# Kernel optimization log

Measured on AMD Instinct MI355X. Metric: run time of the kernel, lower is better.

The kernel has to match this reference:

```python
import jax, jax.numpy as jnp
import numpy as np

B, T, D_MODEL, N_HEADS = 2, 2048, 2048, 16
D_HEAD = D_MODEL // N_HEADS
SCALE = 1.0 / np.sqrt(D_HEAD)


def setup_inputs() -> dict:
    key = jax.random.key(0)
    ks = jax.random.split(key, 5)
    w_std = 1.0 / np.sqrt(D_MODEL)
    x = jax.random.normal(ks[0], (B, T, D_MODEL), dtype=jnp.float32)
    W_q = jax.random.normal(ks[1], (D_MODEL, D_MODEL), dtype=jnp.float32) * w_std
    W_k = jax.random.normal(ks[2], (D_MODEL, D_MODEL), dtype=jnp.float32) * w_std
    W_v = jax.random.normal(ks[3], (D_MODEL, D_MODEL), dtype=jnp.float32) * w_std
    W_o = jax.random.normal(ks[4], (D_MODEL, D_MODEL), dtype=jnp.float32) * w_std
    return {"x": x, "W_q": W_q, "W_k": W_k, "W_v": W_v, "W_o": W_o}


def _split_heads(y):
    # [B, T, D] -> [B, H, T, d_head]
    b, t, _ = y.shape
    return y.reshape(b, t, N_HEADS, D_HEAD).transpose(0, 2, 1, 3)


def reference(x, W_q, W_k, W_v, W_o):
    # Linear layers (torch nn.Linear: y = x @ W.T)
    Q = _split_heads(x @ W_q.T)
    K = _split_heads(x @ W_k.T)
    V = _split_heads(x @ W_v.T)
    # Causal softmax attention (math-equivalent to the tiled online-softmax loop)
    scores = jnp.einsum('bhqd,bhkd->bhqk', Q, K) * SCALE
    causal_mask = jnp.tril(jnp.ones((T, T), dtype=bool))  # [T, T]
    scores = jnp.where(causal_mask, scores, -jnp.inf)
    P = jax.nn.softmax(scores, axis=-1)
    O = jnp.einsum('bhqk,bhkd->bhqd', P, V)
    out = O.transpose(0, 2, 1, 3).reshape(B, T, D_MODEL)  # merge heads
    return out @ W_o.T
```

## Files before the change

### kernel.cpp

```cpp
#include <hip/hip_runtime.h>
#include <hip/hip_bf16.h>
#include <hip/hip_fp16.h>

#define B_   2
#define T_   2048
#define DM   2048
#define NH   16
#define DH   128
#define M_   (B_*T_)
#define SCALE_ 0.08838834764831845f

typedef _Float16 f16;
typedef f16  half8 __attribute__((ext_vector_type(8)));
typedef f16  half4 __attribute__((ext_vector_type(4)));
typedef float f32x4 __attribute__((ext_vector_type(4)));

#define GL16(gp, lp) __builtin_amdgcn_global_load_lds( \
    (const __attribute__((address_space(1))) void*)(gp), \
    (__attribute__((address_space(3))) void*)(lp), 16, 0, 0)

#define MFMA16(a, b, c) __builtin_amdgcn_mfma_f32_16x16x32_f16((a), (b), (c), 0, 0, 0)

struct CvtArgs { const float* s[5]; f16* d[5]; };

__global__ __launch_bounds__(256) void convert_all(CvtArgs a) {
    size_t i4 = (size_t)blockIdx.x * 256 + threadIdx.x;
    int r; size_t off;
    if (i4 < 2097152) { r = 0; off = i4; }
    else { size_t k = i4 - 2097152; r = 1 + (int)(k >> 20); off = k & 1048575; }
    float4 v = *((const float4*)a.s[r] + off);
    half4 h;
    h[0] = (f16)v.x; h[1] = (f16)v.y; h[2] = (f16)v.z; h[3] = (f16)v.w;
    *((half4*)a.d[r] + off) = h;
}

#define NTQ 64

__global__ __launch_bounds__(512, 4)
void qkv3(const f16* __restrict__ A, const f16* __restrict__ Bw,
          f16* __restrict__ dst)
{
    __shared__ __align__(16) char smem[49152];

    const int tid  = threadIdx.x;
    const int lane = tid & 63;
    const int w    = tid >> 6;
    const int wr   = w >> 1, wc = w & 1;

    const int id = (blockIdx.x & 7) * 96 + (blockIdx.x >> 3);
    const int bm = id & 15, bn = id >> 4;
    const int m0 = bm * 256, n0 = bn * 128;

    const int scol8 = (((tid & 3) ^ ((tid >> 2) & 3)) << 3);
    const int rca = (lane & 15) * 64 + ((((lane >> 4) ^ lane) & 3) << 4);

    f32x4 acc[4][4] = {};

#define QA(bufb, s, kt) GL16( \
    A + (size_t)(m0 + (s)*128 + (tid>>2)) * 2048 + (kt)*32 + scol8, \
    smem + (bufb)*24576 + (s)*8192 + w*1024)
#define QB(bufb, kt) GL16( \
    Bw + (size_t)(n0 + (tid>>2)) * 2048 + (kt)*32 + scol8, \
    smem + (bufb)*24576 + 16384 + w*1024)

    QA(0, 0, 0); QA(0, 1, 0); QB(0, 0);

    for (int t = 0; t < NTQ; ++t) {
        const int c = t & 1;
        const char* buf = smem + c * 24576;

        asm volatile("s_waitcnt vmcnt(0)" ::: "memory");
        __builtin_amdgcn_s_barrier();
        __builtin_amdgcn_sched_barrier(0);

        if (t + 1 < NTQ) {
            QA(c ^ 1, 0, t + 1); QA(c ^ 1, 1, t + 1); QB(c ^ 1, t + 1);
        }

        half8 af[4], bf[4];
        #pragma unroll
        for (int m = 0; m < 4; ++m)
            af[m] = *(const half8*)(buf + wr * 4096 + m * 1024 + rca);
        #pragma unroll
        for (int n = 0; n < 4; ++n)
            bf[n] = *(const half8*)(buf + 16384 + wc * 4096 + n * 1024 + rca);

        __builtin_amdgcn_s_setprio(1);
        #pragma unroll
        for (int m = 0; m < 4; ++m)
            #pragma unroll
            for (int n = 0; n < 4; ++n)
                acc[m][n] = MFMA16(af[m], bf[n], acc[m][n]);
        __builtin_amdgcn_s_setprio(0);
    }
#undef QA
#undef QB

    #pragma unroll
    for (int m = 0; m < 4; ++m)
        #pragma unroll
        for (int n = 0; n < 4; ++n)
            #pragma unroll
            for (int j = 0; j < 4; ++j) {
                int row  = m0 + wr * 64 + m * 16 + (lane >> 4) * 4 + j;
                int gcol = n0 + wc * 64 + n * 16 + (lane & 15);
                int sec = gcol >> 11, cic = gcol & 2047;
                int b = row >> 11, tt = row & (T_ - 1);
                int h = cic >> 7, d = cic & 127;
                float cs = (sec == 0) ? SCALE_ : 1.0f;
                dst[(size_t)sec * ((size_t)M_ * 2048) +
                    ((size_t)(b * NH + h) * T_ + tt) * DH + d] = (f16)(acc[m][n][j] * cs);
            }
}

#define NT_K 32

__global__ __launch_bounds__(512, 4)
void wo2(const f16* __restrict__ A, const f16* __restrict__ Bw,
         float* __restrict__ Cf)
{
    __shared__ __align__(16) char smem[65536];

    const int tid  = threadIdx.x;
    const int lane = tid & 63;
    const int w    = tid >> 6;
    const int wr   = w >> 2, wc = w & 3;

    const int id = (blockIdx.x & 7) * 64 + (blockIdx.x >> 3);
    const int bm = id & 31, bn = id >> 5;
    const int m0 = bm * 128, n0 = bn * 128;

    const int scol8 = (((tid & 7) ^ ((tid >> 3) & 7)) << 3);
    const int rc0 = (((lane >> 4) * 16)      ) ^ ((lane & 7) << 4);
    const int rc1 = (64 + (lane >> 4) * 16   ) ^ ((lane & 7) << 4);

    f32x4 acc[4][2] = {};

#define WSTAGE_A(bufb, s, kt) GL16( \
    A + (size_t)(m0 + (tid>>8)*64 + (s)*32 + ((tid>>3)&31)) * 2048 + (kt)*64 + scol8, \
    smem + (bufb)*32768 + (s)*8192 + w*1024)
#define WSTAGE_B(bufb, u, kt) GL16( \
    Bw + (size_t)(n0 + (tid>>7)*32 + (u)*16 + ((tid>>3)&15)) * 2048 + (kt)*64 + scol8, \
    smem + (bufb)*32768 + 16384 + (u)*8192 + w*1024)

    WSTAGE_A(0, 0, 0); WSTAGE_A(0, 1, 0);
    WSTAGE_B(0, 0, 0); WSTAGE_B(0, 1, 0);

    const int abase = wr * 4096 + (lane & 15) * 128;
    const int bbase = 16384 + (wc * 16 + (lane & 15)) * 128;

    for (int t = 0; t < NT_K; ++t) {
        const int c  = t & 1;
        const char* buf = smem + c * 32768;
        const int kt = (t + 1 < NT_K) ? t + 1 : t;

        half8 af[4][2], bfr[2];
        asm volatile("s_waitcnt vmcnt(1)" ::: "memory");
        __builtin_amdgcn_s_barrier();
        __builtin_amdgcn_sched_barrier(0);
        #pragma unroll
        for (int m = 0; m < 4; ++m) {
            const char* p = buf + (m >> 1) * 8192 + abase + (m & 1) * 2048;
            af[m][0] = *(const half8*)(p + rc0);
            af[m][1] = *(const half8*)(p + rc1);
        }
        { const char* p = buf + bbase;
          bfr[0] = *(const half8*)(p + rc0); bfr[1] = *(const half8*)(p + rc1); }
        WSTAGE_A(c ^ 1, 0, kt); WSTAGE_A(c ^ 1, 1, kt);
        __builtin_amdgcn_s_setprio(1);
        #pragma unroll
        for (int m = 0; m < 4; ++m) {
            acc[m][0] = MFMA16(af[m][0], bfr[0], acc[m][0]);
            acc[m][0] = MFMA16(af[m][1], bfr[1], acc[m][0]);
        }
        __builtin_amdgcn_s_setprio(0);

        asm volatile("s_waitcnt vmcnt(2)" ::: "memory");
        __builtin_amdgcn_s_barrier();
        __builtin_amdgcn_sched_barrier(0);
        { const char* p = buf + bbase + 8192;
          bfr[0] = *(const half8*)(p + rc0); bfr[1] = *(const half8*)(p + rc1); }
        WSTAGE_B(c ^ 1, 0, kt); WSTAGE_B(c ^ 1, 1, kt);
        __builtin_amdgcn_s_setprio(1);
        #pragma unroll
        for (int m = 0; m < 4; ++m) {
            acc[m][1] = MFMA16(af[m][0], bfr[0], acc[m][1]);
            acc[m][1] = MFMA16(af[m][1], bfr[1], acc[m][1]);
        }
        __builtin_amdgcn_s_setprio(0);
        __builtin_amdgcn_s_barrier();
    }
#undef WSTAGE_A
#undef WSTAGE_B

    asm volatile("s_waitcnt vmcnt(0)" ::: "memory");

    #pragma unroll
    for (int m = 0; m < 4; ++m)
        #pragma unroll
        for (int u = 0; u < 2; ++u)
            #pragma unroll
            for (int j = 0; j < 4; ++j) {
                int row = m0 + wr * 64 + m * 16 + (lane >> 4) * 4 + j;
                int col = n0 + wc * 32 + u * 16 + (lane & 15);
                Cf[(size_t)row * 2048 + col] = acc[m][u][j];
            }
}

__global__ __launch_bounds__(256)
void vtrans(const f16* __restrict__ Vin, f16* __restrict__ Vout)
{
    __shared__ f16 ld[64][72];
    const int tid = threadIdx.x;
    const int dd = blockIdx.x;
    const int tt = blockIdx.y;
    const int bh = blockIdx.z;

    const int r  = tid >> 2;
    const int s2 = (tid & 3) * 2;

    const f16* src = Vin + ((size_t)bh * T_ + tt * 64 + r) * DH + dd * 64;
    half8 v0 = *(const half8*)(src + s2 * 8);
    half8 v1 = *(const half8*)(src + s2 * 8 + 8);
    #pragma unroll
    for (int e = 0; e < 8; ++e) ld[s2 * 8 + e][r]     = v0[e];
    #pragma unroll
    for (int e = 0; e < 8; ++e) ld[s2 * 8 + 8 + e][r] = v1[e];
    __syncthreads();

    f16* dst = Vout + ((size_t)bh * DH + dd * 64 + r) * T_ + tt * 64;
    *(half8*)(dst + s2 * 8)     = *(const half8*)&ld[r][s2 * 8];
    *(half8*)(dst + s2 * 8 + 8) = *(const half8*)&ld[r][s2 * 8 + 8];
}

#define QB 64
#define KB 64
#define PP 72
#define NQT (T_/QB)

__global__ __launch_bounds__(256, 4)
void attn_fwd(const f16* __restrict__ Q, const f16* __restrict__ K,
              const f16* __restrict__ Vt, f16* __restrict__ O)
{
    __shared__ __align__(16) char Ks[2][16384];
    __shared__ __align__(16) char Vs[2][16384];
    __shared__ __align__(16) f16 Ps[4][16][PP];

    const int tid  = threadIdx.x;
    const int lane = tid & 63;
    const int w    = tid >> 6;
    const int g    = lane >> 4;

    const int bid  = blockIdx.x;
    const int swz  = (bid & 7) * 64 + (bid >> 3);
    const int bh   = swz >> 4;
    const int pair = swz & 15;
    const size_t base = (size_t)bh * T_ * DH;
    const int b = bh >> 4, h = bh & 15;

    const int krow0 = w * 4 + g;
    const int kswz  = ((lane & 15) ^ (krow0 & 7)) << 3;
    const int vrow0 = w * 8 + (lane >> 3);
    const int vswz  = (((lane & 7) ^ ((lane >> 3) & 7)) << 3);

#define STAGE_K(c_, kv) do { \
    _Pragma("unroll") for (int i_ = 0; i_ < 4; ++i_) { \
        const f16* g_ = K + base + (size_t)((kv) + i_*16 + krow0) * DH + kswz; \
        GL16(g_, &Ks[c_][i_*4096 + w*1024]); } } while (0)
#define STAGE_V(c_, kv) do { \
    _Pragma("unroll") for (int i_ = 0; i_ < 4; ++i_) { \
        const f16* g_ = Vt + base + (size_t)(i_*32 + vrow0) * T_ + (kv) + vswz; \
        GL16(g_, &Vs[c_][i_*4096 + w*1024]); } } while (0)

    #pragma unroll
    for (int hf = 0; hf < 2; ++hf) {
        const int qt = (hf == 0) ? pair : (NQT - 1 - pair);
        const int q0 = qt * QB;
        const int ntiles = qt + 1;
        const int qg = q0 + w * 16 + (lane & 15);

        half8 qf[4];
        #pragma unroll
        for (int kk = 0; kk < 4; ++kk)
            qf[kk] = *reinterpret_cast<const half8*>(
                &Q[base + (size_t)qg * DH + kk * 32 + g * 8]);

        float mrun = -1e30f, lrun = 0.f;
        f32x4 o[8] = {};

        __syncthreads();
        STAGE_K(0, 0);
        STAGE_V(0, 0);

        for (int it = 0; it < ntiles; ++it) {
            const int c = it & 1;
            __syncthreads();
            if (it + 1 < ntiles) {
                STAGE_K(c ^ 1, (it + 1) * KB);
                STAGE_V(c ^ 1, (it + 1) * KB);
            }

            const char* kb = &Ks[c][0];
            f32x4 sacc[4] = {};
            __builtin_amdgcn_s_setprio(1);
            #pragma unroll
            for (int n = 0; n < 4; ++n)
                #pragma unroll
                for (int kk = 0; kk < 4; ++kk) {
                    half8 kfv = *(const half8*)(kb + (n*16 + (lane & 15)) * 256 +
                        ((kk*32 + g * 8) * 2 ^ ((lane & 7) << 4)));
                    sacc[n] = MFMA16(kfv, qf[kk], sacc[n]);
                }
            __builtin_amdgcn_s_setprio(0);

            if (it == ntiles - 1) {
                #pragma unroll
                for (int n = 0; n < 4; ++n)
                    #pragma unroll
                    for (int j = 0; j < 4; ++j) {
                        int kg = it * KB + n*16 + g*4 + j;
                        if (kg > qg) sacc[n][j] = -1e30f;
                    }
            }

            float mx = sacc[0][0];
            #pragma unroll
            for (int n = 0; n < 4; ++n)
                #pragma unroll
                for (int j = 0; j < 4; ++j) mx = fmaxf(mx, sacc[n][j]);
            mx = fmaxf(mx, __shfl_xor(mx, 16));
            mx = fmaxf(mx, __shfl_xor(mx, 32));
            float mnew = fmaxf(mrun, mx);
            float sf = __expf(mrun - mnew);
            float rs = 0.f;
            #pragma unroll
            for (int n = 0; n < 4; ++n)
                #pragma unroll
                for (int j = 0; j < 4; ++j) {
                    float p = __expf(sacc[n][j] - mnew);
                    sacc[n][j] = p;
                    rs += p;
                }
            rs += __shfl_xor(rs, 16);
            rs += __shfl_xor(rs, 32);
            lrun = lrun * sf + rs;
            mrun = mnew;
            #pragma unroll
            for (int nn = 0; nn < 8; ++nn) o[nn] *= sf;

            #pragma unroll
            for (int n = 0; n < 4; ++n) {
                half4 hv;
                hv[0] = (f16)sacc[n][0]; hv[1] = (f16)sacc[n][1];
                hv[2] = (f16)sacc[n][2]; hv[3] = (f16)sacc[n][3];
                *reinterpret_cast<half4*>(&Ps[w][lane & 15][n*16 + g*4]) = hv;
            }

            half8 bp[2];
            #pragma unroll
            for (int cc = 0; cc < 2; ++cc)
                bp[cc] = *reinterpret_cast<const half8*>(&Ps[w][lane & 15][cc*32 + g*8]);

            const char* vb = &Vs[c][0];
            __builtin_amdgcn_s_setprio(1);
            #pragma unroll
            for (int n = 0; n < 8; ++n)
                #pragma unroll
                for (int cc = 0; cc < 2; ++cc) {
                    half8 vf = *(const half8*)(vb + (n*16 + (lane & 15)) * 128 +
                        ((cc*64 + g*16) ^ ((lane & 7) << 4)));
                    o[n] = MFMA16(vf, bp[cc], o[n]);
                }
            __builtin_amdgcn_s_setprio(0);
        }

        float invl = 1.0f / lrun;
        #pragma unroll
        for (int n = 0; n < 8; ++n) {
            half4 hv;
            hv[0] = (f16)(o[n][0] * invl); hv[1] = (f16)(o[n][1] * invl);
            hv[2] = (f16)(o[n][2] * invl); hv[3] = (f16)(o[n][3] * invl);
            *reinterpret_cast<half4*>(
                &O[((size_t)(b * T_ + qg) * NH + h) * DH + n*16 + g*4]) = hv;
        }
    }
#undef STAGE_K
#undef STAGE_V
}

extern "C" void kernel_launch(void* const* d_in, const int* in_sizes, int n_in,
                              void* d_out, int out_size, void* d_ws, size_t ws_size,
                              hipStream_t stream)
{
    const float* x  = (const float*)d_in[0];
    const float* wq = (const float*)d_in[1];
    const float* wk = (const float*)d_in[2];
    const float* wv = (const float*)d_in[3];
    const float* wo = (const float*)d_in[4];
    float* out = (float*)d_out;

    const size_t nx = (size_t)M_ * DM;
    const size_t nw = (size_t)DM * DM;
    const size_t need = (nx * 5 + nw * 4) * sizeof(f16);
    if (ws_size < need) return;

    char* ws = (char*)d_ws;
    f16* xh  = (f16*)ws;  ws += nx * 2;
    f16* wqh = (f16*)ws;  ws += nw * 2;
    f16* wkh = (f16*)ws;  ws += nw * 2;
    f16* wvh = (f16*)ws;  ws += nw * 2;
    f16* woh = (f16*)ws;  ws += nw * 2;
    f16* Qh  = (f16*)ws;  ws += nx * 2;
    f16* Kh  = (f16*)ws;  ws += nx * 2;
    f16* Vh  = (f16*)ws;  ws += nx * 2;
    f16* Oh  = (f16*)ws;  ws += nx * 2;

    f16* Vth = xh;

    CvtArgs ca;
    ca.s[0] = x;  ca.d[0] = xh;
    ca.s[1] = wq; ca.d[1] = wqh;
    ca.s[2] = wk; ca.d[2] = wkh;
    ca.s[3] = wv; ca.d[3] = wvh;
    ca.s[4] = wo; ca.d[4] = woh;
    convert_all<<<24576, 256, 0, stream>>>(ca);

    qkv3<<<dim3(768), 512, 0, stream>>>(xh, wqh, Qh);

    vtrans<<<dim3(2, 32, 32), 256, 0, stream>>>(Vh, Vth);

    attn_fwd<<<dim3(512), 256, 0, stream>>>(Qh, Kh, Vth, Oh);

    wo2<<<dim3(512), 512, 0, stream>>>(Oh, woh, out);
}
```

Measured before the change: 256.7 us.

## Restructure QKV GEMM to 256x192 tiles with K=64 stages and interleaved prefetch

The fused QKV projection kernel moves from 256x128 output tiles with K=32 steps to 256x192 tiles with K=64 steps, cutting the grid from 768 to 512 blocks and raising reuse of each loaded A tile. The main loop is software-pipelined: next-stage global-to-LDS loads are split into chunks and interleaved with MFMA groups behind partial vmcnt waits, and fragments for the next stage are read from LDS ahead of use. The cost is a much larger LDS footprint (112 KB) and more registers, so occupancy drops to 2 blocks per CU, and 512 blocks may leave the wave tail uneven.

```diff
diff --git a/kernel.cpp b/kernel.cpp
--- a/kernel.cpp
+++ b/kernel.cpp
@@ -34,86 +34,155 @@
     *((half4*)a.d[r] + off) = h;
 }
 
-#define NTQ 64
-
-__global__ __launch_bounds__(512, 4)
+#define NT_K 32
+
+__global__ __launch_bounds__(512, 2)
 void qkv3(const f16* __restrict__ A, const f16* __restrict__ Bw,
           f16* __restrict__ dst)
 {
-    __shared__ __align__(16) char smem[49152];
+    __shared__ __align__(16) char smem[114688];
 
     const int tid  = threadIdx.x;
     const int lane = tid & 63;
     const int w    = tid >> 6;
     const int wr   = w >> 1, wc = w & 1;
 
-    const int id = (blockIdx.x & 7) * 96 + (blockIdx.x >> 3);
+    const int id = (blockIdx.x & 7) * 64 + (blockIdx.x >> 3);
     const int bm = id & 15, bn = id >> 4;
-    const int m0 = bm * 256, n0 = bn * 128;
-
-    const int scol8 = (((tid & 3) ^ ((tid >> 2) & 3)) << 3);
-    const int rca = (lane & 15) * 64 + ((((lane >> 4) ^ lane) & 3) << 4);
-
-    f32x4 acc[4][4] = {};
-
-#define QA(bufb, s, kt) GL16( \
-    A + (size_t)(m0 + (s)*128 + (tid>>2)) * 2048 + (kt)*32 + scol8, \
-    smem + (bufb)*24576 + (s)*8192 + w*1024)
-#define QB(bufb, kt) GL16( \
-    Bw + (size_t)(n0 + (tid>>2)) * 2048 + (kt)*32 + scol8, \
-    smem + (bufb)*24576 + 16384 + w*1024)
-
-    QA(0, 0, 0); QA(0, 1, 0); QB(0, 0);
-
-    for (int t = 0; t < NTQ; ++t) {
-        const int c = t & 1;
-        const char* buf = smem + c * 24576;
-
-        asm volatile("s_waitcnt vmcnt(0)" ::: "memory");
+    const int m0 = bm * 256, n0 = bn * 192;
+
+    const int scol8 = (((tid & 7) ^ ((tid >> 3) & 7)) << 3);
+    const int rc0 = (((lane >> 4) * 16)      ) ^ ((lane & 7) << 4);
+    const int rc1 = (64 + (lane >> 4) * 16   ) ^ ((lane & 7) << 4);
+
+    f32x4 acc[4][6] = {};
+
+#define QSTAGE_A(bufb, ch, s, kt) GL16( \
+    A + (size_t)(m0 + (ch)*128 + (tid>>8)*64 + (s)*32 + ((tid>>3)&31)) * 2048 + (kt)*64 + scol8, \
+    smem + (bufb)*57344 + (ch)*16384 + (s)*8192 + w*1024)
+#define QSTAGE_B(bufb, u, kt) GL16( \
+    Bw + (size_t)(n0 + (tid>>7)*48 + (u)*16 + ((tid>>3)&15)) * 2048 + (kt)*64 + scol8, \
+    smem + (bufb)*57344 + 32768 + (u)*8192 + w*1024)
+
+    const int abase = (wr >> 1) * 16384 + (wr & 1) * 4096 + (lane & 15) * 128;
+    const int bbase = 32768 + wc * 4096 + (lane & 15) * 128;
+
+    half8 af0[4][2], af1[4][2], bnx[2];
+
+    QSTAGE_A(0, 0, 0, 0); QSTAGE_A(0, 0, 1, 0);
+    QSTAGE_A(0, 1, 0, 0); QSTAGE_A(0, 1, 1, 0);
+    QSTAGE_B(0, 0, 0);    QSTAGE_B(0, 1, 0);    QSTAGE_B(0, 2, 0);
+    {
+        asm volatile("s_waitcnt vmcnt(2)" ::: "memory");
         __builtin_amdgcn_s_barrier();
         __builtin_amdgcn_sched_barrier(0);
-
-        if (t + 1 < NTQ) {
-            QA(c ^ 1, 0, t + 1); QA(c ^ 1, 1, t + 1); QB(c ^ 1, t + 1);
+        const char* buf0 = smem;
+        #pragma unroll
+        for (int m = 0; m < 4; ++m) {
+            const char* p = buf0 + (m >> 1) * 8192 + abase + (m & 1) * 2048;
+            af0[m][0] = *(const half8*)(p + rc0);
+            af0[m][1] = *(const half8*)(p + rc1);
         }
-
-        half8 af[4], bf[4];
-        #pragma unroll
-        for (int m = 0; m < 4; ++m)
-            af[m] = *(const half8*)(buf + wr * 4096 + m * 1024 + rca);
-        #pragma unroll
-        for (int n = 0; n < 4; ++n)
-            bf[n] = *(const half8*)(buf + 16384 + wc * 4096 + n * 1024 + rca);
-
-        __builtin_amdgcn_s_setprio(1);
-        #pragma unroll
-        for (int m = 0; m < 4; ++m)
-            #pragma unroll
-            for (int n = 0; n < 4; ++n)
-                acc[m][n] = MFMA16(af[m], bf[n], acc[m][n]);
-        __builtin_amdgcn_s_setprio(0);
+        bnx[0] = *(const half8*)(buf0 + bbase + rc0);
+        bnx[1] = *(const half8*)(buf0 + bbase + rc1);
     }
-#undef QA
-#undef QB
+
+#define GATE(n_) do { \
+    asm volatile("s_waitcnt vmcnt(" #n_ ")" ::: "memory"); \
+    __builtin_amdgcn_s_barrier(); \
+    __builtin_amdgcn_sched_barrier(0); \
+} while (0)
+
+#define MFC(AF, BB, f_) do { \
+    __builtin_amdgcn_s_setprio(1); \
+    _Pragma("unroll") \
+    for (int m_ = 0; m_ < 4; ++m_) { \
+        acc[m_][f_] = MFMA16(AF[m_][0], (BB)[0], acc[m_][f_]); \
+        acc[m_][f_] = MFMA16(AF[m_][1], (BB)[1], acc[m_][f_]); \
+    } \
+    __builtin_amdgcn_s_setprio(0); \
+} while (0)
+
+#define RDB(dstv, off) do { \
+    const char* p_ = buf + bbase + (off); \
+    dstv[0] = *(const half8*)(p_ + rc0); \
+    dstv[1] = *(const half8*)(p_ + rc1); \
+} while (0)
+
+#define BODY(t_, c_, AFC, AFN) do { \
+    const char* buf  = smem + (c_) * 57344; \
+    const char* nbuf = smem + ((c_) ^ 1) * 57344; \
+    const int  kt    = ((t_) + 1 < NT_K) ? (t_) + 1 : (t_); \
+    half8 b3[2], b1[2], b4[2], b2[2], b5[2]; \
+     \
+    RDB(b3, 2048); \
+    QSTAGE_A((c_) ^ 1, 0, 0, kt); QSTAGE_A((c_) ^ 1, 0, 1, kt); \
+    MFC(AFC, bnx, 0); \
+     \
+    GATE(3); \
+    RDB(b1, 8192); \
+    QSTAGE_A((c_) ^ 1, 1, 0, kt); QSTAGE_A((c_) ^ 1, 1, 1, kt); \
+    MFC(AFC, b3, 3); \
+     \
+    RDB(b4, 8192 + 2048); \
+    QSTAGE_B((c_) ^ 1, 0, kt); \
+    MFC(AFC, b1, 1); \
+     \
+    GATE(5); \
+    RDB(b2, 16384); \
+    QSTAGE_B((c_) ^ 1, 1, kt); \
+    MFC(AFC, b4, 4); \
+     \
+    GATE(1); \
+    RDB(b5, 16384 + 2048); \
+    { const char* p_ = nbuf + abase; \
+      AFN[0][0] = *(const half8*)(p_ + rc0); \
+      AFN[0][1] = *(const half8*)(p_ + rc1); \
+      AFN[1][0] = *(const half8*)(p_ + 2048 + rc0); \
+      AFN[1][1] = *(const half8*)(p_ + 2048 + rc1); } \
+    QSTAGE_B((c_) ^ 1, 2, kt); \
+    MFC(AFC, b2, 2); \
+     \
+    { const char* p_ = nbuf + 8192 + abase; \
+      AFN[2][0] = *(const half8*)(p_ + rc0); \
+      AFN[2][1] = *(const half8*)(p_ + rc1); \
+      AFN[3][0] = *(const half8*)(p_ + 2048 + rc0); \
+      AFN[3][1] = *(const half8*)(p_ + 2048 + rc1); } \
+    { const char* p_ = nbuf + bbase; \
+      bnx[0] = *(const half8*)(p_ + rc0); \
+      bnx[1] = *(const half8*)(p_ + rc1); } \
+    MFC(AFC, b5, 5); \
+} while (0)
+
+    for (int t = 0; t < NT_K; t += 2) {
+        BODY(t,     0, af0, af1);
+        BODY(t + 1, 1, af1, af0);
+    }
+#undef BODY
+#undef RDB
+#undef MFC
+#undef GATE
+#undef QSTAGE_A
+#undef QSTAGE_B
+
+    asm volatile("s_waitcnt vmcnt(0)" ::: "memory");
 
     #pragma unroll
     for (int m = 0; m < 4; ++m)
         #pragma unroll
-        for (int n = 0; n < 4; ++n)
+        for (int f = 0; f < 6; ++f)
             #pragma unroll
             for (int j = 0; j < 4; ++j) {
                 int row  = m0 + wr * 64 + m * 16 + (lane >> 4) * 4 + j;
-                int gcol = n0 + wc * 64 + n * 16 + (lane & 15);
+                int gcol = n0 + wc * 96 + f * 16 + (lane & 15);
                 int sec = gcol >> 11, cic = gcol & 2047;
                 int b = row >> 11, tt = row & (T_ - 1);
                 int h = cic >> 7, d = cic & 127;
                 float cs = (sec == 0) ? SCALE_ : 1.0f;
                 dst[(size_t)sec * ((size_t)M_ * 2048) +
-                    ((size_t)(b * NH + h) * T_ + tt) * DH + d] = (f16)(acc[m][n][j] * cs);
+                    ((size_t)(b * NH + h) * T_ + tt) * DH + d] = (f16)(acc[m][f][j] * cs);
             }
 }
-
-#define NT_K 32
 
 __global__ __launch_bounds__(512, 4)
 void wo2(const f16* __restrict__ A, const f16* __restrict__ Bw,
@@ -425,7 +494,7 @@
     ca.s[4] = wo; ca.d[4] = woh;
     convert_all<<<24576, 256, 0, stream>>>(ca);
 
-    qkv3<<<dim3(768), 512, 0, stream>>>(xh, wqh, Qh);
+    qkv3<<<dim3(512), 512, 0, stream>>>(xh, wqh, Qh);
 
     vtrans<<<dim3(2, 32, 32), 256, 0, stream>>>(Vh, Vth);
 
```

Measured after the change: 234.4 us. 1.09x faster.

## Restructure QKV GEMM into 128x192 tiles with staged interleaved loads and MFMAs

Applied to the files above, without the earlier changes.

The fused QKV projection GEMM moves from 256x128 tiles with 512 threads and K-step 32 to 128x192 tiles with 256 threads and K-step 64. Each wave now owns a 64x96 output block. The next stage's global-to-LDS loads are split into chunks and interleaved with the MFMA groups, using partial vmcnt waits and barriers so loads overlap compute. This raises LDS use to 80KB per block and the accumulator register count per wave, which lowers occupancy.

```diff
diff --git a/kernel.cpp b/kernel.cpp
--- a/kernel.cpp
+++ b/kernel.cpp
@@ -34,86 +34,133 @@
     *((half4*)a.d[r] + off) = h;
 }
 
-#define NTQ 64
-
-__global__ __launch_bounds__(512, 4)
+#define NT_K 32
+
+__global__ __launch_bounds__(256, 2)
 void qkv3(const f16* __restrict__ A, const f16* __restrict__ Bw,
           f16* __restrict__ dst)
 {
-    __shared__ __align__(16) char smem[49152];
+    __shared__ __align__(16) char smem[81920];
 
     const int tid  = threadIdx.x;
     const int lane = tid & 63;
     const int w    = tid >> 6;
     const int wr   = w >> 1, wc = w & 1;
 
-    const int id = (blockIdx.x & 7) * 96 + (blockIdx.x >> 3);
-    const int bm = id & 15, bn = id >> 4;
-    const int m0 = bm * 256, n0 = bn * 128;
-
-    const int scol8 = (((tid & 3) ^ ((tid >> 2) & 3)) << 3);
-    const int rca = (lane & 15) * 64 + ((((lane >> 4) ^ lane) & 3) << 4);
-
-    f32x4 acc[4][4] = {};
-
-#define QA(bufb, s, kt) GL16( \
-    A + (size_t)(m0 + (s)*128 + (tid>>2)) * 2048 + (kt)*32 + scol8, \
-    smem + (bufb)*24576 + (s)*8192 + w*1024)
-#define QB(bufb, kt) GL16( \
-    Bw + (size_t)(n0 + (tid>>2)) * 2048 + (kt)*32 + scol8, \
-    smem + (bufb)*24576 + 16384 + w*1024)
-
-    QA(0, 0, 0); QA(0, 1, 0); QB(0, 0);
-
-    for (int t = 0; t < NTQ; ++t) {
+    const int id = (blockIdx.x & 7) * 128 + (blockIdx.x >> 3);
+    const int bm = id & 31, bn = id >> 5;
+    const int m0 = bm * 128, n0 = bn * 192;
+
+    const int scol8 = (((tid & 7) ^ ((tid >> 3) & 7)) << 3);
+    const int rc0 = (((lane >> 4) * 16)      ) ^ ((lane & 7) << 4);
+    const int rc1 = (64 + (lane >> 4) * 16   ) ^ ((lane & 7) << 4);
+
+    f32x4 acc[4][6] = {};
+
+#define QSA(bufb, s, kt) GL16( \
+    A + (size_t)(m0 + (s)*32 + (tid>>3)) * 2048 + (kt)*64 + scol8, \
+    smem + (bufb)*40960 + (s)*4096 + w*1024)
+#define QSB(bufb, u, kt) GL16( \
+    Bw + (size_t)(n0 + (u)*32 + (tid>>3)) * 2048 + (kt)*64 + scol8, \
+    smem + (bufb)*40960 + 16384 + (u)*4096 + w*1024)
+
+    QSA(0, 0, 0); QSA(0, 1, 0); QSA(0, 2, 0); QSA(0, 3, 0);
+    QSB(0, 0, 0); QSB(0, 3, 0); QSB(0, 1, 0); QSB(0, 4, 0);
+    QSB(0, 2, 0); QSB(0, 5, 0);
+
+    const int abase = wr * 8192 + (lane & 15) * 128;
+    const int bbase = 16384 + wc * 12288 + (lane & 15) * 128;
+
+#define GATE(n_) do { \
+    asm volatile("s_waitcnt vmcnt(" #n_ ")" ::: "memory"); \
+    __builtin_amdgcn_s_barrier(); \
+    __builtin_amdgcn_sched_barrier(0); \
+} while (0)
+
+#define MFC(BB, f_) do { \
+    __builtin_amdgcn_s_setprio(1); \
+    _Pragma("unroll") \
+    for (int m_ = 0; m_ < 4; ++m_) { \
+        acc[m_][f_] = MFMA16(af[m_][0], (BB)[0], acc[m_][f_]); \
+        acc[m_][f_] = MFMA16(af[m_][1], (BB)[1], acc[m_][f_]); \
+    } \
+    __builtin_amdgcn_s_setprio(0); \
+} while (0)
+
+#define RDB(dstv, off) do { \
+    const char* p_ = buf + bbase + (off); \
+    dstv[0] = *(const half8*)(p_ + rc0); \
+    dstv[1] = *(const half8*)(p_ + rc1); \
+} while (0)
+
+    for (int t = 0; t < NT_K; ++t) {
         const int c = t & 1;
-        const char* buf = smem + c * 24576;
-
-        asm volatile("s_waitcnt vmcnt(0)" ::: "memory");
-        __builtin_amdgcn_s_barrier();
-        __builtin_amdgcn_sched_barrier(0);
-
-        if (t + 1 < NTQ) {
-            QA(c ^ 1, 0, t + 1); QA(c ^ 1, 1, t + 1); QB(c ^ 1, t + 1);
-        }
-
-        half8 af[4], bf[4];
-        #pragma unroll
-        for (int m = 0; m < 4; ++m)
-            af[m] = *(const half8*)(buf + wr * 4096 + m * 1024 + rca);
-        #pragma unroll
-        for (int n = 0; n < 4; ++n)
-            bf[n] = *(const half8*)(buf + 16384 + wc * 4096 + n * 1024 + rca);
-
-        __builtin_amdgcn_s_setprio(1);
-        #pragma unroll
-        for (int m = 0; m < 4; ++m)
-            #pragma unroll
-            for (int n = 0; n < 4; ++n)
-                acc[m][n] = MFMA16(af[m], bf[n], acc[m][n]);
-        __builtin_amdgcn_s_setprio(0);
+        const char* buf = smem + c * 40960;
+        const int kt = (t + 1 < NT_K) ? t + 1 : t;
+
+        half8 af[4][2], be[2], bo[2];
+
+        GATE(4);
+
+        #pragma unroll
+        for (int m = 0; m < 4; ++m) {
+            const char* p = buf + abase + m * 2048;
+            af[m][0] = *(const half8*)(p + rc0);
+            af[m][1] = *(const half8*)(p + rc1);
+        }
+        RDB(be, 0);
+        QSA(c ^ 1, 0, kt); QSA(c ^ 1, 1, kt);
+        MFC(be, 0);
+
+        RDB(bo, 2048);
+        QSA(c ^ 1, 2, kt); QSA(c ^ 1, 3, kt);
+        MFC(bo, 1);
+
+        GATE(6);
+
+        RDB(be, 4096);
+        QSB(c ^ 1, 0, kt); QSB(c ^ 1, 3, kt);
+        MFC(be, 2);
+
+        RDB(bo, 6144);
+        QSB(c ^ 1, 1, kt); QSB(c ^ 1, 4, kt);
+        MFC(bo, 3);
+
+        GATE(8);
+
+        RDB(be, 8192);
+        QSB(c ^ 1, 2, kt); QSB(c ^ 1, 5, kt);
+        MFC(be, 4);
+
+        RDB(bo, 10240);
+        MFC(bo, 5);
     }
-#undef QA
-#undef QB
+#undef RDB
+#undef MFC
+#undef GATE
+#undef QSA
+#undef QSB
+
+    asm volatile("s_waitcnt vmcnt(0)" ::: "memory");
 
     #pragma unroll
     for (int m = 0; m < 4; ++m)
         #pragma unroll
-        for (int n = 0; n < 4; ++n)
+        for (int f = 0; f < 6; ++f)
             #pragma unroll
             for (int j = 0; j < 4; ++j) {
                 int row  = m0 + wr * 64 + m * 16 + (lane >> 4) * 4 + j;
-                int gcol = n0 + wc * 64 + n * 16 + (lane & 15);
+                int gcol = n0 + wc * 96 + f * 16 + (lane & 15);
                 int sec = gcol >> 11, cic = gcol & 2047;
                 int b = row >> 11, tt = row & (T_ - 1);
                 int h = cic >> 7, d = cic & 127;
                 float cs = (sec == 0) ? SCALE_ : 1.0f;
                 dst[(size_t)sec * ((size_t)M_ * 2048) +
-                    ((size_t)(b * NH + h) * T_ + tt) * DH + d] = (f16)(acc[m][n][j] * cs);
+                    ((size_t)(b * NH + h) * T_ + tt) * DH + d] = (f16)(acc[m][f][j] * cs);
             }
 }
 
-#define NT_K 32
+#define NT_W 32
 
 __global__ __launch_bounds__(512, 4)
 void wo2(const f16* __restrict__ A, const f16* __restrict__ Bw,
@@ -149,10 +196,10 @@
     const int abase = wr * 4096 + (lane & 15) * 128;
     const int bbase = 16384 + (wc * 16 + (lane & 15)) * 128;
 
-    for (int t = 0; t < NT_K; ++t) {
+    for (int t = 0; t < NT_W; ++t) {
         const int c  = t & 1;
         const char* buf = smem + c * 32768;
-        const int kt = (t + 1 < NT_K) ? t + 1 : t;
+        const int kt = (t + 1 < NT_W) ? t + 1 : t;
 
         half8 af[4][2], bfr[2];
         asm volatile("s_waitcnt vmcnt(1)" ::: "memory");
@@ -425,7 +472,7 @@
     ca.s[4] = wo; ca.d[4] = woh;
     convert_all<<<24576, 256, 0, stream>>>(ca);
 
-    qkv3<<<dim3(768), 512, 0, stream>>>(xh, wqh, Qh);
+    qkv3<<<dim3(1024), 256, 0, stream>>>(xh, wqh, Qh);
 
     vtrans<<<dim3(2, 32, 32), 256, 0, stream>>>(Vh, Vth);
 
```

Result: faster. 239.5 us (-6.7%).
